# Kernel optimization log

Measured on AMD Instinct MI355X. Metric: run time of the kernel, lower is better.

The kernel has to match this reference:

```python
import jax, jax.numpy as jnp
import numpy as np

NEG = -10000.0
PAD_ID = 0


def setup_inputs() -> dict:
    key = jax.random.key(0)
    ks = jax.random.split(key, 9)
    B, S, D, K, L = 32, 256, 512, 8, 64
    word_rep = jax.random.normal(ks[0], (B, S, D), jnp.float32)
    mask = jnp.ones((B, S), jnp.int32)
    # conv_w[k,:,:,:k+1] are the taps of Conv1d(D, D, k+1); padded to width K for a single tensor
    conv_w = jax.random.normal(ks[1], (K, D, D, K), jnp.float32) * 0.02
    conv_b = jax.random.normal(ks[2], (K, D), jnp.float32) * 0.02
    cls_w = jax.random.normal(ks[3], (L, D), jnp.float32) * 0.02
    cls_b = jax.random.normal(ks[4], (L,), jnp.float32) * 0.02
    T = jax.random.normal(ks[5], (L, L), jnp.float32) * 0.01
    T = T.at[PAD_ID, :].set(NEG).at[:, PAD_ID].set(NEG)
    T_from_BEGIN = jax.random.normal(ks[6], (L,), jnp.float32) * 0.01
    T_from_BEGIN = T_from_BEGIN.at[PAD_ID].set(NEG)
    T_to_END = jax.random.normal(ks[7], (L,), jnp.float32) * 0.01
    T_to_END = T_to_END.at[PAD_ID].set(NEG)
    return dict(word_rep=word_rep, mask=mask, conv_w=conv_w, conv_b=conv_b,
                cls_w=cls_w, cls_b=cls_b, T=T, T_from_BEGIN=T_from_BEGIN, T_to_END=T_to_END)


def _semicrf(word_rep, mask, conv_w, conv_b, cls_w, cls_b, T, T_from_BEGIN, T_to_END):
    B, S, D = word_rep.shape
    K = conv_w.shape[0]
    L = cls_w.shape[0]
    # ---- segment representations: Conv1d(D, D, k+1) placed at [:, k:, k, :] ----
    x = jnp.transpose(word_rep, (0, 2, 1))  # [B, D, S]
    word_seq_rep = jnp.zeros((B, S, K, D), word_rep.dtype)
    for k in range(K):
        w = conv_w[k, :, :, :k + 1]  # [D_out, D_in, k+1]
        out = jax.lax.conv_general_dilated(
            x, w, window_strides=(1,), padding='VALID',
            dimension_numbers=('NCH', 'OIH', 'NCH')) + conv_b[k][None, :, None]  # [B, D, S-k]
        word_seq_rep = word_seq_rep.at[:, k:, k, :].set(jnp.transpose(out, (0, 2, 1)))
    # ---- label scores ----
    label_score = jnp.einsum('bskd,ld->bskl', word_seq_rep, cls_w) + cls_b  # [B,S,K,L]
    label_score = label_score.at[..., PAD_ID].set(NEG)
    seg_ok = jnp.arange(K)[None, :] <= jnp.arange(S)[:, None]  # [S, K]: segment of len k+1 valid only if t >= k
    mask3 = (mask[:, :, None] == 1) & seg_ok[None]              # [B, S, K]
    label_score = jnp.where(mask3[..., None], label_score, NEG)
    # ---- semi-CRF forward recursion over t (sequential scan) ----
    # buf[:, j] holds log_alpha at position t-1-j for j in [0, K)
    def step(buf, inp):
        ls_t, m_t, t = inp  # [B,K,L], [B,K], scalar
        lse_prev = jax.nn.logsumexp(buf, axis=2)                                  # over kk -> [B,K,L']
        tmp = jax.nn.logsumexp(T[None, None, :, :] + lse_prev[:, :, None, :], axis=3)  # over l' -> [B,K,L]
        rec = jnp.where(m_t[..., None], ls_t + tmp, NEG)
        begin = ls_t + T_from_BEGIN[None, None, :]
        karr = jnp.arange(K)[None, :, None]
        row = jnp.where(karr == t, begin, jnp.where(karr > t, NEG, rec))  # [B,K,L]
        buf = jnp.concatenate([row[:, None], buf[:, :-1]], axis=1)
        return buf, row

    buf0 = jnp.full((B, K, K, L), NEG, word_rep.dtype)
    xs = (jnp.transpose(label_score, (1, 0, 2, 3)), jnp.transpose(mask3, (1, 0, 2)), jnp.arange(S))
    _, rows = jax.lax.scan(step, buf0, xs)
    log_alpha = jnp.concatenate(
        [jnp.transpose(rows, (1, 0, 2, 3)), jnp.full((B, 1, K, L), NEG, word_rep.dtype)], axis=1)  # [B,S+1,K,L]
    # ---- log partition: gather log_alpha at last token per segment length, add T_to_END, logsumexp ----
    lengths = jnp.sum(mask, axis=1)                                   # [B]
    idxs = lengths[:, None] - (jnp.arange(K)[None, :] + 1)            # [B,K]
    idxs = jnp.where(idxs >= 0, idxs, S - 1)
    idx_arr = jnp.broadcast_to(idxs[:, None, :, None], (B, 1, K, L))
    g = jnp.take_along_axis(log_alpha, idx_arr, axis=1)[:, 0]         # [B,K,L]
    scores = g + T_to_END[None, None, :]
    return jax.nn.logsumexp(scores.reshape(B, K * L), axis=1)         # [B]


def reference(word_rep, mask, conv_w, conv_b, cls_w, cls_b, T, T_from_BEGIN, T_to_END):
    return _semicrf(word_rep, mask, conv_w, conv_b, cls_w, cls_b, T, T_from_BEGIN, T_to_END)
```

## Files before the change

kernel.cpp:

```cpp
#include <hip/hip_runtime.h>
#include <hip/hip_bf16.h>

#define NEGV (-10000.0f)
constexpr int B_ = 32, S_ = 256, D_ = 512, K_ = 8, L_ = 64;

typedef __bf16 bf16_t;
typedef bf16_t bf16x8 __attribute__((ext_vector_type(8)));
typedef float f32x4 __attribute__((ext_vector_type(4)));

__device__ __forceinline__ float u2f(unsigned int u) {
  union { unsigned int u; float f; } x; x.u = u; return x.f;
}
__device__ __forceinline__ unsigned int f2bfbits(float f) {
  union { bf16_t h; unsigned short u; } x; x.h = (bf16_t)f; return (unsigned int)x.u;
}

__global__ __launch_bounds__(256) void cast_kernel(const float* __restrict__ wr,
                                                   bf16_t* __restrict__ Awr,
                                                   const float* __restrict__ cls_w,
                                                   bf16_t* __restrict__ clsb) {
  const int bid = blockIdx.x;
  if (bid < 2048) {
    const int i = (bid * 256 + threadIdx.x) * 8;
    const float4 a = *(const float4*)(wr + i);
    const float4 b = *(const float4*)(wr + i + 4);
    bf16x8 o;
    o[0] = (bf16_t)a.x; o[1] = (bf16_t)a.y; o[2] = (bf16_t)a.z; o[3] = (bf16_t)a.w;
    o[4] = (bf16_t)b.x; o[5] = (bf16_t)b.y; o[6] = (bf16_t)b.z; o[7] = (bf16_t)b.w;
    *(bf16x8*)(Awr + i) = o;
  } else {
    const int i = ((bid - 2048) * 256 + threadIdx.x) * 8;
    const float4 a = *(const float4*)(cls_w + i);
    const float4 b = *(const float4*)(cls_w + i + 4);
    bf16x8 o;
    o[0] = (bf16_t)a.x; o[1] = (bf16_t)a.y; o[2] = (bf16_t)a.z; o[3] = (bf16_t)a.w;
    o[4] = (bf16_t)b.x; o[5] = (bf16_t)b.y; o[6] = (bf16_t)b.z; o[7] = (bf16_t)b.w;
    *(bf16x8*)(clsb + i) = o;
  }
}

__global__ __launch_bounds__(256) void w2_kernel(const float* __restrict__ conv_w,
                                                 const bf16_t* __restrict__ clsb,
                                                 bf16_t* __restrict__ Vt) {
  const int k = blockIdx.y;
  const int m0 = blockIdx.x * 128;
  const int tid = threadIdx.x;
  const int w = tid >> 6, lane = tid & 63;
  const int wm = w & 1, wn = w >> 1;
  const int lrow = lane & 15, quad = lane >> 4;
  const float* A = conv_w + (size_t)k * 2097152;
  f32x4 acc[4][2] = {};
#pragma unroll 2
  for (int kk = 0; kk < 16; kk++) {
    const int d0 = kk * 32 + quad * 8;
    const bf16x8 b0 = *(const bf16x8*)(clsb + (wn * 32 + lrow) * 512 + kk * 32 + quad * 8);
    const bf16x8 b1 = *(const bf16x8*)(clsb + (wn * 32 + 16 + lrow) * 512 + kk * 32 + quad * 8);
#pragma unroll
    for (int mi = 0; mi < 4; mi++) {
      const int ih = m0 + wm * 64 + mi * 16 + lrow;
      const float* ap = A + (size_t)d0 * 4096 + ih;
      bf16x8 a;
      a[0] = (bf16_t)ap[0 * 4096]; a[1] = (bf16_t)ap[1 * 4096];
      a[2] = (bf16_t)ap[2 * 4096]; a[3] = (bf16_t)ap[3 * 4096];
      a[4] = (bf16_t)ap[4 * 4096]; a[5] = (bf16_t)ap[5 * 4096];
      a[6] = (bf16_t)ap[6 * 4096]; a[7] = (bf16_t)ap[7 * 4096];
      acc[mi][0] = __builtin_amdgcn_mfma_f32_16x16x32_bf16(a, b0, acc[mi][0], 0, 0, 0);
      acc[mi][1] = __builtin_amdgcn_mfma_f32_16x16x32_bf16(a, b1, acc[mi][1], 0, 0, 0);
    }
  }
#pragma unroll
  for (int mi = 0; mi < 4; mi++) {
#pragma unroll
    for (int dd = 0; dd < 4; dd++) {
      const int ih = m0 + wm * 64 + mi * 16 + quad * 4 + dd;
      const int i = ih >> 3, h = ih & 7;
      const int o = k - h;
      if (o >= 0) {
#pragma unroll
        for (int ni = 0; ni < 2; ni++) {
          const int l = wn * 32 + ni * 16 + lrow;
          Vt[(size_t)(k * 64 + l) * 4096 + o * 512 + i] = (bf16_t)acc[mi][ni][dd];
        }
      }
    }
  }
}

__global__ __launch_bounds__(256) void bias2_kernel(const float* __restrict__ conv_b,
                                                    const float* __restrict__ cls_w,
                                                    const float* __restrict__ cls_b,
                                                    float* __restrict__ bias2) {
  const int k = blockIdx.x;
  const int tid = threadIdx.x;
  const int l = tid & 63, c = tid >> 6;
  __shared__ float partb[4][64];
  float s = 0.f;
  for (int d = c * 128; d < c * 128 + 128; d++)
    s += conv_b[k * D_ + d] * cls_w[l * D_ + d];
  partb[c][l] = s;
  __syncthreads();
  if (tid < 64)
    bias2[k * 64 + tid] = cls_b[tid] + partb[0][tid] + partb[1][tid] + partb[2][tid] + partb[3][tid];
}

__global__ __launch_bounds__(256) void ls_mfma(const bf16_t* __restrict__ Awr,
                                               const bf16_t* __restrict__ Vt,
                                               const float* __restrict__ bias2,
                                               const int* __restrict__ mask,
                                               unsigned int* __restrict__ ELSd) {
  constexpr int LDA = 520;
  __shared__ __align__(16) bf16_t As[71 * LDA];
  const int tid = threadIdx.x;
  const int m0 = blockIdx.x * 64;
  const int y = blockIdx.y;
  const int w = tid >> 6, lane = tid & 63;
  const int lrow = lane & 15, quad = lane >> 4;
  const int tblA[4] = {7, 0, 5, 2}, tblB[4] = {6, 1, 4, 3};
  const int kS = (y == 0) ? tblA[w] : tblB[w];

  for (int c = tid; c < 71 * 64; c += 256) {
    const int row = c >> 6, col8 = c & 63;
    int src = m0 - 7 + row;
    if (src < 0) src = 0;
    const uint4 v = *(const uint4*)(Awr + (size_t)src * 512 + col8 * 8);
    *(uint4*)(&As[row * LDA + col8 * 8]) = v;
  }
  __syncthreads();

  f32x4 acc[4][4] = {};
  const int NJ = 16 * (kS + 1);
  const bf16_t* vbase = Vt + (size_t)(kS * 64 + lrow) * 4096 + quad * 8;
#pragma unroll 2
  for (int j = 0; j < NJ; j++) {
    const int o = j >> 4;
    const int col = (j & 15) * 32;
    bf16x8 bfr[4];
#pragma unroll
    for (int ni = 0; ni < 4; ni++)
      bfr[ni] = *(const bf16x8*)(vbase + (size_t)(ni * 16) * 4096 + j * 32);
    const int abase = (lrow + 7 - o) * LDA + col + quad * 8;
#pragma unroll
    for (int mi = 0; mi < 4; mi++) {
      const bf16x8 a = *(const bf16x8*)(&As[abase + mi * 16 * LDA]);
#pragma unroll
      for (int ni = 0; ni < 4; ni++)
        acc[mi][ni] = __builtin_amdgcn_mfma_f32_16x16x32_bf16(a, bfr[ni], acc[mi][ni], 0, 0, 0);
    }
  }

  __syncthreads();
  unsigned short* buf = (unsigned short*)As;
#pragma unroll
  for (int ni = 0; ni < 4; ni++) {
    const int l = ni * 16 + lrow;
    const float bn = bias2[kS * 64 + l];
#pragma unroll
    for (int mi = 0; mi < 4; mi++) {
#pragma unroll
      for (int d = 0; d < 4; d++) {
        const int ml = mi * 16 + quad * 4 + d;
        const int m = m0 + ml;
        const int t = m & 255;
        const bool mok = (mask[m] == 1) && (t >= kS) && (l != 0);
        const float e = mok ? __expf(acc[mi][ni][d] + bn) : 0.f;
        buf[w * 4096 + ml * 64 + l] = (unsigned short)f2bfbits(e);
      }
    }
  }
  __syncthreads();
#pragma unroll
  for (int g = 0; g < 2; g++) {
    const int plane = g * 2 + y;
    const unsigned short* lo = buf + (g * 2) * 4096;
    const unsigned short* hi = buf + (g * 2 + 1) * 4096;
#pragma unroll
    for (int it = 0; it < 16; it++) {
      const int idx = it * 256 + tid;
      const unsigned int dw = (unsigned int)lo[idx] | ((unsigned int)hi[idx] << 16);
      ELSd[((size_t)plane * 8192 + m0 + (idx >> 6)) * 64 + (idx & 63)] = dw;
    }
  }
}

__global__ __launch_bounds__(256, 1) void dp_kernel(const float* __restrict__ T,
                                                    const float* __restrict__ Tfb_g,
                                                    const unsigned int* __restrict__ ELSd,
                                                    float* __restrict__ Mg_lin,
                                                    float* __restrict__ cs_g) {
  const int b = blockIdx.x, tid = threadIdx.x;
  const int w = tid >> 6, l = tid & 63;
  __shared__ __align__(16) float ebuf[64];
  __shared__ float part[4][72];
  __shared__ __align__(16) float pmax[4];
  f32x4 rTq[4];
#pragma unroll
  for (int q = 0; q < 4; q++) {
#pragma unroll
    for (int e = 0; e < 4; e++) rTq[q][e] = __expf(T[l * 64 + w * 16 + q * 4 + e]);
  }
  float mh0 = 0.f, mh1 = 0.f, mh2 = 0.f, mh3 = 0.f, mh4 = 0.f, mh5 = 0.f, mh6 = 0.f, mh7 = 0.f;
  float c = 0.f;
  const unsigned int* e0p = ELSd + ((size_t)0 * 8192 + b * 256) * 64 + l;
  const unsigned int* e1p = ELSd + ((size_t)1 * 8192 + b * 256) * 64 + l;
  const unsigned int* e2p = ELSd + ((size_t)2 * 8192 + b * 256) * 64 + l;
  const unsigned int* e3p = ELSd + ((size_t)3 * 8192 + b * 256) * 64 + l;
  uint4 r0, r1, r2, r3;
  if (w == 0) {
    mh0 = __expf(Tfb_g[l]);
    r0 = make_uint4(e0p[0 * 64], e1p[0 * 64], e2p[0 * 64], e3p[0 * 64]);
    r1 = make_uint4(e0p[1 * 64], e1p[1 * 64], e2p[1 * 64], e3p[1 * 64]);
    r2 = make_uint4(e0p[2 * 64], e1p[2 * 64], e2p[2 * 64], e3p[2 * 64]);
    r3 = make_uint4(e0p[3 * 64], e1p[3 * 64], e2p[3 * 64], e3p[3 * 64]);
  }
  for (int t4 = 0; t4 < 256; t4 += 4) {
#pragma unroll
    for (int u = 0; u < 4; u++) {
      const int t = t4 + u;
      if (w == 0) {
        if (t > 0) {
          const float p0 = part[0][l], p1 = part[1][l], p2 = part[2][l], p3 = part[3][l];
          const float m4 = (p0 + p1) + (p2 + p3);
          if ((t & 3) == 0) {
            const f32x4 pm = *(const f32x4*)pmax;
            float S = fmaxf(fmaxf(pm[0], pm[1]), fmaxf(pm[2], pm[3]));
            S = fmaxf(S, 1e-30f);
            const float inv = __builtin_amdgcn_rcpf(S);
            c += __logf(S);
            mh7 = mh6 * inv; mh6 = mh5 * inv; mh5 = mh4 * inv; mh4 = mh3 * inv;
            mh3 = mh2 * inv; mh2 = mh1 * inv; mh1 = mh0 * inv; mh0 = m4 * inv;
          } else {
            mh7 = mh6; mh6 = mh5; mh5 = mh4; mh4 = mh3;
            mh3 = mh2; mh2 = mh1; mh1 = mh0; mh0 = m4;
          }
        }
        const uint4 q = (u == 0) ? r0 : (u == 1) ? r1 : (u == 2) ? r2 : r3;
        const float f7 = u2f(q.x << 16), fk0 = u2f(q.x & 0xFFFF0000u);
        const float f6 = u2f(q.y << 16), fk1 = u2f(q.y & 0xFFFF0000u);
        const float f5 = u2f(q.z << 16), fk2 = u2f(q.z & 0xFFFF0000u);
        const float f4 = u2f(q.w << 16), fk3 = u2f(q.w & 0xFFFF0000u);
        const float e = ((fk0 * mh0 + fk1 * mh1) + (fk2 * mh2 + fk3 * mh3)) +
                        ((f4 * mh4 + f5 * mh5) + (f6 * mh6 + f7 * mh7));
        ebuf[l] = e;
        int nt = t + 4; if (nt > 255) nt = 255;
        const uint4 nv = make_uint4(e0p[(size_t)nt * 64], e1p[(size_t)nt * 64],
                                    e2p[(size_t)nt * 64], e3p[(size_t)nt * 64]);
        if (u == 0) r0 = nv; else if (u == 1) r1 = nv; else if (u == 2) r2 = nv; else r3 = nv;
      } else if (w == 1) {
        if (t > 0) {
          const float p0 = part[0][l], p1 = part[1][l], p2 = part[2][l], p3 = part[3][l];
          const float m4 = (p0 + p1) + (p2 + p3);
          Mg_lin[((size_t)b * 256 + (t - 1)) * 64 + l] = m4;
          if (l == 0) cs_g[b * 256 + (t - 1)] = c;
          if ((t & 3) == 0) {
            const f32x4 pm = *(const f32x4*)pmax;
            float S = fmaxf(fmaxf(pm[0], pm[1]), fmaxf(pm[2], pm[3]));
            S = fmaxf(S, 1e-30f);
            c += __logf(S);
          }
        }
      }
      __syncthreads();
      {
        const f32x4* evp = (const f32x4*)ebuf;
        const f32x4 v0 = evp[w * 4 + 0], v1 = evp[w * 4 + 1];
        const f32x4 v2 = evp[w * 4 + 2], v3 = evp[w * 4 + 3];
        f32x4 s01 = rTq[0] * v0 + rTq[1] * v1;
        f32x4 s23 = rTq[2] * v2 + rTq[3] * v3;
        const f32x4 sv = s01 + s23;
        part[w][l] = (sv[0] + sv[1]) + (sv[2] + sv[3]);
        const f32x4 mx = __builtin_elementwise_max(__builtin_elementwise_max(v0, v1),
                                                   __builtin_elementwise_max(v2, v3));
        if (l == 0) pmax[w] = fmaxf(fmaxf(mx[0], mx[1]), fmaxf(mx[2], mx[3]));
      }
      __syncthreads();
    }
  }
  if (w == 1) {
    const float p0 = part[0][l], p1 = part[1][l], p2 = part[2][l], p3 = part[3][l];
    const float m4 = (p0 + p1) + (p2 + p3);
    Mg_lin[((size_t)b * 256 + 255) * 64 + l] = m4;
    if (l == 0) cs_g[b * 256 + 255] = c;
  }
}

__global__ __launch_bounds__(64) void final_kernel(const int* __restrict__ mask,
                                                   const float* __restrict__ Tfb_g,
                                                   const float* __restrict__ T2e_g,
                                                   const unsigned int* __restrict__ ELSd,
                                                   const float* __restrict__ Mg_lin,
                                                   const float* __restrict__ cs_g,
                                                   float* __restrict__ out) {
  const int b = blockIdx.x, lane = threadIdx.x;
  int lenp = 0;
  for (int s = lane; s < S_; s += 64) lenp += (mask[b * S_ + s] == 1) ? 1 : 0;
#pragma unroll
  for (int off = 32; off > 0; off >>= 1) lenp += __shfl_xor(lenp, off);
  const int len = lenp;
  const float t2e = T2e_g[lane];
  float vals[8];
  float mx = -3.4e38f;
#pragma unroll
  for (int k = 0; k < 8; k++) {
    int tk = len - 1 - k;
    if (tk < 0) tk = S_ - 1;
    float g;
    if (k > tk) {
      g = NEGV;
    } else {
      const int p = (k < 4) ? k : (7 - k);
      const unsigned int dw = ELSd[((size_t)p * 8192 + b * 256 + tk) * 64 + lane];
      const float elsv = (k < 4) ? u2f(dw & 0xFFFF0000u) : u2f(dw << 16);
      const float ls = (elsv > 0.f) ? __logf(elsv) : NEGV;
      if (k == tk) {
        g = ls + Tfb_g[lane];
      } else if (mask[b * S_ + tk] == 1) {
        const int u = tk - 1 - k;
        const float mlin = Mg_lin[((size_t)b * S_ + u) * 64 + lane];
        const float M = (mlin > 0.f) ? (__logf(mlin) + cs_g[b * S_ + u]) : -1e30f;
        g = ls + M;
      } else {
        g = NEGV;
      }
    }
    const float v = g + t2e;
    vals[k] = v;
    mx = fmaxf(mx, v);
  }
#pragma unroll
  for (int off = 32; off > 0; off >>= 1) mx = fmaxf(mx, __shfl_xor(mx, off));
  float s = 0.f;
#pragma unroll
  for (int k = 0; k < 8; k++) s += __expf(vals[k] - mx);
#pragma unroll
  for (int off = 32; off > 0; off >>= 1) s += __shfl_xor(s, off);
  if (lane == 0) out[b] = __logf(s) + mx;
}

extern "C" void kernel_launch(void* const* d_in, const int* in_sizes, int n_in,
                              void* d_out, int out_size, void* d_ws, size_t ws_size,
                              hipStream_t stream) {
  const float* wr     = (const float*)d_in[0];
  const int*   mask   = (const int*)d_in[1];
  const float* conv_w = (const float*)d_in[2];
  const float* conv_b = (const float*)d_in[3];
  const float* cls_w  = (const float*)d_in[4];
  const float* cls_b  = (const float*)d_in[5];
  const float* T      = (const float*)d_in[6];
  const float* Tfb    = (const float*)d_in[7];
  const float* T2e    = (const float*)d_in[8];
  float* out = (float*)d_out;

  float* ws = (float*)d_ws;
  bf16_t* Vt    = (bf16_t*)ws;
  bf16_t* Awr   = (bf16_t*)(ws + 1048576);
  float*  bias2 = ws + 3145728;
  unsigned int* ELSd = (unsigned int*)(ws + 3146240);
  float*  Mg    = ws + 5243392;
  float*  cs    = ws + 5767680;
  bf16_t* clsb  = (bf16_t*)(ws + 5775872);

  cast_kernel<<<2064, 256, 0, stream>>>(wr, Awr, cls_w, clsb);
  w2_kernel<<<dim3(32, 8), 256, 0, stream>>>(conv_w, clsb, Vt);
  bias2_kernel<<<8, 256, 0, stream>>>(conv_b, cls_w, cls_b, bias2);
  ls_mfma<<<dim3(128, 2), 256, 0, stream>>>(Awr, Vt, bias2, mask, ELSd);
  dp_kernel<<<32, 256, 0, stream>>>(T, Tfb, ELSd, Mg, cs);
  final_kernel<<<32, 64, 0, stream>>>(mask, Tfb, T2e, ELSd, Mg, cs, out);
}
```

Measured before the change: 303.0 us.

## Collapse semi-CRF DP kernel to a single wavefront without block barriers

The DP recurrence kernel now runs with one 64-lane wavefront per batch element instead of four cooperating waves. Each lane holds a full row of exp(T) in registers and does the 64-wide matvec itself from LDS, so the two __syncthreads per timestep and the partial-sum exchange go away. The block max used for rescaling is now a wavefront shuffle reduction, and Mg/cs writes are done inline. The trade is four times more FMAs per lane on a serial critical path and higher register pressure, in exchange for removing barrier latency.

```diff
diff --git a/kernel.cpp b/kernel.cpp
--- a/kernel.cpp
+++ b/kernel.cpp
@@ -182,104 +182,90 @@
   }
 }
 
-__global__ __launch_bounds__(256, 1) void dp_kernel(const float* __restrict__ T,
-                                                    const float* __restrict__ Tfb_g,
-                                                    const unsigned int* __restrict__ ELSd,
-                                                    float* __restrict__ Mg_lin,
-                                                    float* __restrict__ cs_g) {
-  const int b = blockIdx.x, tid = threadIdx.x;
-  const int w = tid >> 6, l = tid & 63;
+__global__ __launch_bounds__(64) void dp_kernel(const float* __restrict__ T,
+                                                const float* __restrict__ Tfb_g,
+                                                const unsigned int* __restrict__ ELSd,
+                                                float* __restrict__ Mg_lin,
+                                                float* __restrict__ cs_g) {
+  const int b = blockIdx.x;
+  const int l = threadIdx.x;
   __shared__ __align__(16) float ebuf[64];
-  __shared__ float part[4][72];
-  __shared__ __align__(16) float pmax[4];
-  f32x4 rTq[4];
-#pragma unroll
-  for (int q = 0; q < 4; q++) {
-#pragma unroll
-    for (int e = 0; e < 4; e++) rTq[q][e] = __expf(T[l * 64 + w * 16 + q * 4 + e]);
-  }
-  float mh0 = 0.f, mh1 = 0.f, mh2 = 0.f, mh3 = 0.f, mh4 = 0.f, mh5 = 0.f, mh6 = 0.f, mh7 = 0.f;
-  float c = 0.f;
+
+  f32x4 rTv[16];
+#pragma unroll
+  for (int jj = 0; jj < 16; jj++) {
+    const float4 tv = *(const float4*)(T + l * 64 + jj * 4);
+    rTv[jj][0] = __expf(tv.x);
+    rTv[jj][1] = __expf(tv.y);
+    rTv[jj][2] = __expf(tv.z);
+    rTv[jj][3] = __expf(tv.w);
+  }
+
   const unsigned int* e0p = ELSd + ((size_t)0 * 8192 + b * 256) * 64 + l;
   const unsigned int* e1p = ELSd + ((size_t)1 * 8192 + b * 256) * 64 + l;
   const unsigned int* e2p = ELSd + ((size_t)2 * 8192 + b * 256) * 64 + l;
   const unsigned int* e3p = ELSd + ((size_t)3 * 8192 + b * 256) * 64 + l;
-  uint4 r0, r1, r2, r3;
-  if (w == 0) {
-    mh0 = __expf(Tfb_g[l]);
-    r0 = make_uint4(e0p[0 * 64], e1p[0 * 64], e2p[0 * 64], e3p[0 * 64]);
-    r1 = make_uint4(e0p[1 * 64], e1p[1 * 64], e2p[1 * 64], e3p[1 * 64]);
-    r2 = make_uint4(e0p[2 * 64], e1p[2 * 64], e2p[2 * 64], e3p[2 * 64]);
-    r3 = make_uint4(e0p[3 * 64], e1p[3 * 64], e2p[3 * 64], e3p[3 * 64]);
-  }
+
+  float mh0 = __expf(Tfb_g[l]);
+  float mh1 = 0.f, mh2 = 0.f, mh3 = 0.f, mh4 = 0.f, mh5 = 0.f, mh6 = 0.f, mh7 = 0.f;
+  float c = 0.f;
+  float m4 = 0.f;
+  float S_next = 0.f;
+
+  uint4 r0 = make_uint4(e0p[0 * 64], e1p[0 * 64], e2p[0 * 64], e3p[0 * 64]);
+  uint4 r1 = make_uint4(e0p[1 * 64], e1p[1 * 64], e2p[1 * 64], e3p[1 * 64]);
+  uint4 r2 = make_uint4(e0p[2 * 64], e1p[2 * 64], e2p[2 * 64], e3p[2 * 64]);
+  uint4 r3 = make_uint4(e0p[3 * 64], e1p[3 * 64], e2p[3 * 64], e3p[3 * 64]);
+
   for (int t4 = 0; t4 < 256; t4 += 4) {
 #pragma unroll
     for (int u = 0; u < 4; u++) {
       const int t = t4 + u;
-      if (w == 0) {
-        if (t > 0) {
-          const float p0 = part[0][l], p1 = part[1][l], p2 = part[2][l], p3 = part[3][l];
-          const float m4 = (p0 + p1) + (p2 + p3);
-          if ((t & 3) == 0) {
-            const f32x4 pm = *(const f32x4*)pmax;
-            float S = fmaxf(fmaxf(pm[0], pm[1]), fmaxf(pm[2], pm[3]));
-            S = fmaxf(S, 1e-30f);
-            const float inv = __builtin_amdgcn_rcpf(S);
-            c += __logf(S);
-            mh7 = mh6 * inv; mh6 = mh5 * inv; mh5 = mh4 * inv; mh4 = mh3 * inv;
-            mh3 = mh2 * inv; mh2 = mh1 * inv; mh1 = mh0 * inv; mh0 = m4 * inv;
-          } else {
-            mh7 = mh6; mh6 = mh5; mh5 = mh4; mh4 = mh3;
-            mh3 = mh2; mh2 = mh1; mh1 = mh0; mh0 = m4;
-          }
+      if (t > 0) {
+        if ((t & 3) == 0) {
+          const float S = fmaxf(S_next, 1e-30f);
+          const float inv = __builtin_amdgcn_rcpf(S);
+          c += __logf(S);
+          mh7 = mh6 * inv; mh6 = mh5 * inv; mh5 = mh4 * inv; mh4 = mh3 * inv;
+          mh3 = mh2 * inv; mh2 = mh1 * inv; mh1 = mh0 * inv; mh0 = m4 * inv;
+        } else {
+          mh7 = mh6; mh6 = mh5; mh5 = mh4; mh4 = mh3;
+          mh3 = mh2; mh2 = mh1; mh1 = mh0; mh0 = m4;
         }
-        const uint4 q = (u == 0) ? r0 : (u == 1) ? r1 : (u == 2) ? r2 : r3;
-        const float f7 = u2f(q.x << 16), fk0 = u2f(q.x & 0xFFFF0000u);
-        const float f6 = u2f(q.y << 16), fk1 = u2f(q.y & 0xFFFF0000u);
-        const float f5 = u2f(q.z << 16), fk2 = u2f(q.z & 0xFFFF0000u);
-        const float f4 = u2f(q.w << 16), fk3 = u2f(q.w & 0xFFFF0000u);
-        const float e = ((fk0 * mh0 + fk1 * mh1) + (fk2 * mh2 + fk3 * mh3)) +
-                        ((f4 * mh4 + f5 * mh5) + (f6 * mh6 + f7 * mh7));
-        ebuf[l] = e;
-        int nt = t + 4; if (nt > 255) nt = 255;
+      }
+      const uint4 q = (u == 0) ? r0 : (u == 1) ? r1 : (u == 2) ? r2 : r3;
+      const float f7 = u2f(q.x << 16), fk0 = u2f(q.x & 0xFFFF0000u);
+      const float f6 = u2f(q.y << 16), fk1 = u2f(q.y & 0xFFFF0000u);
+      const float f5 = u2f(q.z << 16), fk2 = u2f(q.z & 0xFFFF0000u);
+      const float f4 = u2f(q.w << 16), fk3 = u2f(q.w & 0xFFFF0000u);
+      const float e = ((fk0 * mh0 + fk1 * mh1) + (fk2 * mh2 + fk3 * mh3)) +
+                      ((f4 * mh4 + f5 * mh5) + (f6 * mh6 + f7 * mh7));
+      ebuf[l] = e;
+      asm volatile("s_waitcnt lgkmcnt(0)" ::: "memory");
+
+      {
+        int nt = t + 4;
+        if (nt > 255) nt = 255;
         const uint4 nv = make_uint4(e0p[(size_t)nt * 64], e1p[(size_t)nt * 64],
                                     e2p[(size_t)nt * 64], e3p[(size_t)nt * 64]);
         if (u == 0) r0 = nv; else if (u == 1) r1 = nv; else if (u == 2) r2 = nv; else r3 = nv;
-      } else if (w == 1) {
-        if (t > 0) {
-          const float p0 = part[0][l], p1 = part[1][l], p2 = part[2][l], p3 = part[3][l];
-          const float m4 = (p0 + p1) + (p2 + p3);
-          Mg_lin[((size_t)b * 256 + (t - 1)) * 64 + l] = m4;
-          if (l == 0) cs_g[b * 256 + (t - 1)] = c;
-          if ((t & 3) == 0) {
-            const f32x4 pm = *(const f32x4*)pmax;
-            float S = fmaxf(fmaxf(pm[0], pm[1]), fmaxf(pm[2], pm[3]));
-            S = fmaxf(S, 1e-30f);
-            c += __logf(S);
-          }
-        }
-      }
-      __syncthreads();
-      {
-        const f32x4* evp = (const f32x4*)ebuf;
-        const f32x4 v0 = evp[w * 4 + 0], v1 = evp[w * 4 + 1];
-        const f32x4 v2 = evp[w * 4 + 2], v3 = evp[w * 4 + 3];
-        f32x4 s01 = rTq[0] * v0 + rTq[1] * v1;
-        f32x4 s23 = rTq[2] * v2 + rTq[3] * v3;
-        const f32x4 sv = s01 + s23;
-        part[w][l] = (sv[0] + sv[1]) + (sv[2] + sv[3]);
-        const f32x4 mx = __builtin_elementwise_max(__builtin_elementwise_max(v0, v1),
-                                                   __builtin_elementwise_max(v2, v3));
-        if (l == 0) pmax[w] = fmaxf(fmaxf(mx[0], mx[1]), fmaxf(mx[2], mx[3]));
-      }
-      __syncthreads();
-    }
-  }
-  if (w == 1) {
-    const float p0 = part[0][l], p1 = part[1][l], p2 = part[2][l], p3 = part[3][l];
-    const float m4 = (p0 + p1) + (p2 + p3);
-    Mg_lin[((size_t)b * 256 + 255) * 64 + l] = m4;
-    if (l == 0) cs_g[b * 256 + 255] = c;
+      }
+      if ((t & 3) == 3) {
+        float pm = e;
+#pragma unroll
+        for (int off = 32; off > 0; off >>= 1) pm = fmaxf(pm, __shfl_xor(pm, off));
+        S_next = pm;
+      }
+
+      f32x4 acc = {0.f, 0.f, 0.f, 0.f};
+      const f32x4* ev = (const f32x4*)ebuf;
+#pragma unroll
+      for (int jj = 0; jj < 16; jj++) acc += rTv[jj] * ev[jj];
+      m4 = (acc[0] + acc[1]) + (acc[2] + acc[3]);
+
+      Mg_lin[((size_t)b * 256 + t) * 64 + l] = m4;
+      if (l == 0) cs_g[b * 256 + t] = c;
+    }
   }
 }
 
@@ -363,6 +349,6 @@
   w2_kernel<<<dim3(32, 8), 256, 0, stream>>>(conv_w, clsb, Vt);
   bias2_kernel<<<8, 256, 0, stream>>>(conv_b, cls_w, cls_b, bias2);
   ls_mfma<<<dim3(128, 2), 256, 0, stream>>>(Awr, Vt, bias2, mask, ELSd);
-  dp_kernel<<<32, 256, 0, stream>>>(T, Tfb, ELSd, Mg, cs);
+  dp_kernel<<<32, 64, 0, stream>>>(T, Tfb, ELSd, Mg, cs);
   final_kernel<<<32, 64, 0, stream>>>(mask, Tfb, T2e, ELSd, Mg, cs, out);
 }
```

Result: no change. 307.4 us (+1.5%).
